# Kernel tuning notes

Measured on AMD Instinct MI355X. Metric: run time of the kernel, lower is better.

The kernel has to match this reference:

```python
import jax, jax.numpy as jnp
import numpy as np

TOKENS = 32768
DIM = 2048
N_EXPERTS = 64
TOP_K = 6
ROUTE_SCALE = 1.0


def setup_inputs() -> dict:
    key = jax.random.key(0)
    k1, k2, k3 = jax.random.split(key, 3)
    x = jax.random.normal(k1, (TOKENS, DIM), dtype=jnp.float32)
    weight = jax.random.normal(k2, (N_EXPERTS, DIM), dtype=jnp.float32) * (1.0 / np.sqrt(DIM))
    bias = jax.random.normal(k3, (N_EXPERTS,), dtype=jnp.float32) * 0.01
    return {"x": x, "weight": weight, "bias": bias}


def reference(x, weight, bias):
    # scores = F.linear(x, weight): [T, E]
    logits = jnp.einsum('td,ed->te', x, weight)
    # softmax in float32 (score_func == 'softmax')
    original_scores = jax.nn.softmax(logits.astype(jnp.float32), axis=-1)
    # bias only affects expert selection, not the returned weights
    biased = original_scores + bias
    _, indices = jax.lax.top_k(biased, TOP_K)  # [T, top_k]
    weights = jnp.take_along_axis(original_scores, indices, axis=-1)
    weights = weights * ROUTE_SCALE
    return weights.astype(x.dtype), indices
```

## Files before the change

kernel.cpp:

```cpp
#include <hip/hip_runtime.h>
#include <hip/hip_bf16.h>
#include <math.h>

#define TOKENS 32768
#define DIM    2048
#define NEXP   64
#define TOPK   6

#define BM   64
#define BK   64
#define NIT  (DIM / BK)
#define PL_SH   (NEXP * BK)
#define CH_SH   (3 * PL_SH)
#define CH_B    (CH_SH * 2)

typedef float f32x4 __attribute__((ext_vector_type(4)));
typedef short sh8  __attribute__((ext_vector_type(8)));

__device__ __forceinline__ ushort f2bf(float f) {
    union { __hip_bfloat16 b; ushort u; } c;
    c.b = __float2bfloat16(f);
    return c.u;
}
__device__ __forceinline__ float bf2f(ushort u) {
    union { ushort u; __hip_bfloat16 b; } c;
    c.u = u;
    return __bfloat162float(c.b);
}

#define GLDS(gp, lp) __builtin_amdgcn_global_load_lds( \
    (const __attribute__((address_space(1))) void*)(gp), \
    (__attribute__((address_space(3))) void*)(lp), 16, 0, 0)

__global__ void wsplit_kernel(const float* __restrict__ w, short* __restrict__ ws)
{
    const int idx = blockIdx.x * 256 + threadIdx.x;
    const int g  = idx & 7;
    const int e  = (idx >> 3) & 63;
    const int it = idx >> 9;
    const int c  = g ^ (e & 7);

    const float* src = w + (long)e * DIM + it * BK + c * 8;
    float4 f0 = *(const float4*)(src);
    float4 f1 = *(const float4*)(src + 4);

    sh8 h, m, l;
#pragma unroll
    for (int i = 0; i < 8; ++i) {
        float f = (i < 4) ? ((const float*)&f0)[i] : ((const float*)&f1)[i - 4];
        ushort hh = f2bf(f);  float r1 = f - bf2f(hh);
        ushort mm = f2bf(r1); float r2 = r1 - bf2f(mm);
        ushort ll = f2bf(r2);
        h[i] = (short)hh; m[i] = (short)mm; l[i] = (short)ll;
    }
    short* dst = ws + (long)it * CH_SH + e * BK + g * 8;
    *(sh8*)(dst)              = h;
    *(sh8*)(dst + PL_SH)      = m;
    *(sh8*)(dst + 2 * PL_SH)  = l;
}

__global__ __launch_bounds__(256, 2)
void gate_kernel(const float* __restrict__ x,
                 const short* __restrict__ ws,
                 const float* __restrict__ bias,
                 float* __restrict__ out)
{
    __shared__ __align__(16) short smem[2 * CH_SH];

    const int tid  = threadIdx.x;
    const int wave = tid >> 6;
    const int lane = tid & 63;
    const int quad = lane >> 4;
    const int l15  = lane & 15;
    const int tok0 = blockIdx.x * BM;

    const float* xg = x + (long)(tok0 + wave * 16 + l15) * DIM + quad * 8;

    const int h8  = l15 & 7;
    const int vb0 = l15 * 128 + (((0 * 4 + quad) ^ h8) << 4);
    const int vb1 = l15 * 128 + (((1 * 4 + quad) ^ h8) << 4);
    const char* sb = (const char*)smem;

    f32x4 acc[4];
#pragma unroll
    for (int nt = 0; nt < 4; ++nt) acc[nt] = (f32x4){0.f, 0.f, 0.f, 0.f};

    auto stage = [&](int it, int bp) {
        const short* s = ws + (long)it * CH_SH + tid * 8;
        short* d = smem + bp * CH_SH + tid * 8;
#pragma unroll
        for (int j = 0; j < 6; ++j) GLDS(s + j * 2048, d + j * 2048);
    };

    float4 fA[4], fB[4];
    auto loadA = [&](float4* f, int it) {
        const float* p = xg + it * BK;
        f[0] = *(const float4*)(p);
        f[1] = *(const float4*)(p + 4);
        f[2] = *(const float4*)(p + 32);
        f[3] = *(const float4*)(p + 36);
    };

    sh8 fr[2][3];
    auto convert = [&](const float4* f) {
#pragma unroll
        for (int ks = 0; ks < 2; ++ks) {
            sh8 h, m, l;
#pragma unroll
            for (int i = 0; i < 8; ++i) {
                float v = ((const float*)&f[ks * 2])[i];
                ushort hh = f2bf(v);  float r1 = v - bf2f(hh);
                ushort mm = f2bf(r1); float r2 = r1 - bf2f(mm);
                h[i] = (short)hh; m[i] = (short)mm; l[i] = (short)f2bf(r2);
            }
            fr[ks][0] = h; fr[ks][1] = m; fr[ks][2] = l;
        }
    };

    auto compute = [&](int bufbyte) {
#pragma unroll
        for (int ks = 0; ks < 2; ++ks) {
            const int va = (ks ? vb1 : vb0) + bufbyte;
#pragma unroll
            for (int nt = 0; nt < 4; ++nt) {
                const int ro = va + nt * 2048;
                sh8 bh = *(const sh8*)(sb + ro);
                sh8 bm = *(const sh8*)(sb + ro + 8192);
                sh8 bl = *(const sh8*)(sb + ro + 16384);
                acc[nt] = __builtin_amdgcn_mfma_f32_16x16x32_bf16(fr[ks][0], bh, acc[nt], 0, 0, 0);
                acc[nt] = __builtin_amdgcn_mfma_f32_16x16x32_bf16(fr[ks][1], bh, acc[nt], 0, 0, 0);
                acc[nt] = __builtin_amdgcn_mfma_f32_16x16x32_bf16(fr[ks][0], bm, acc[nt], 0, 0, 0);
                acc[nt] = __builtin_amdgcn_mfma_f32_16x16x32_bf16(fr[ks][2], bh, acc[nt], 0, 0, 0);
                acc[nt] = __builtin_amdgcn_mfma_f32_16x16x32_bf16(fr[ks][1], bm, acc[nt], 0, 0, 0);
                acc[nt] = __builtin_amdgcn_mfma_f32_16x16x32_bf16(fr[ks][0], bl, acc[nt], 0, 0, 0);
            }
        }
    };

    stage(0, 0);
    loadA(fA, 0);
    loadA(fB, 1);
    __syncthreads();

#pragma unroll 1
    for (int it = 0; it < NIT; it += 2) {
        stage(it + 1, 1);
        convert(fA);
        if (it + 2 < NIT) loadA(fA, it + 2);
        compute(0);
        __syncthreads();

        if (it + 2 < NIT) stage(it + 2, 0);
        convert(fB);
        if (it + 3 < NIT) loadA(fB, it + 3);
        compute(CH_B);
        __syncthreads();
    }

    float* red = (float*)smem;
#pragma unroll
    for (int nt = 0; nt < 4; ++nt)
#pragma unroll
        for (int j = 0; j < 4; ++j) {
            const int row = wave * 16 + quad * 4 + j;
            const int col = nt * 16 + l15;
            red[row * 69 + col] = acc[nt][j];
        }
    __syncthreads();

    {
        const int t = lane >> 2;
        const int s = lane & 3;
        const int row = wave * 16 + t;

        float lg[16];
#pragma unroll
        for (int i = 0; i < 16; ++i) lg[i] = red[row * 69 + s * 16 + i];

        float mx = lg[0];
#pragma unroll
        for (int i = 1; i < 16; ++i) mx = fmaxf(mx, lg[i]);
        mx = fmaxf(mx, __shfl_xor(mx, 1));
        mx = fmaxf(mx, __shfl_xor(mx, 2));

        float sum = 0.f;
#pragma unroll
        for (int i = 0; i < 16; ++i) { lg[i] = __expf(lg[i] - mx); sum += lg[i]; }
        sum += __shfl_xor(sum, 1);
        sum += __shfl_xor(sum, 2);
        const float inv = 1.0f / sum;

        float sc[16], bz[16];
#pragma unroll
        for (int i = 0; i < 16; ++i) {
            sc[i] = lg[i] * inv;
            bz[i] = sc[i] + bias[s * 16 + i];
        }

        const int tok = tok0 + wave * 16 + t;
        float* wout = out + (long)tok * TOPK;
        float* iout = out + (long)TOKENS * TOPK + (long)tok * TOPK;

        unsigned used = 0;
#pragma unroll
        for (int p = 0; p < TOPK; ++p) {
            float bv = -INFINITY; int bi = 1 << 20; float bw = 0.f;
#pragma unroll
            for (int i = 0; i < 16; ++i) {
                float v = ((used >> i) & 1u) ? -INFINITY : bz[i];
                if (v > bv) { bv = v; bi = s * 16 + i; bw = sc[i]; }
            }
#pragma unroll
            for (int d = 1; d < 4; d <<= 1) {
                float ov = __shfl_xor(bv, d);
                int   oi = __shfl_xor(bi, d);
                float ow = __shfl_xor(bw, d);
                if (ov > bv || (ov == bv && oi < bi)) { bv = ov; bi = oi; bw = ow; }
            }
            if ((bi >> 4) == s) used |= 1u << (bi & 15);
            if (s == 0) { wout[p] = bw; iout[p] = (float)bi; }
        }
    }
}

extern "C" void kernel_launch(void* const* d_in, const int* in_sizes, int n_in,
                              void* d_out, int out_size, void* d_ws, size_t ws_size,
                              hipStream_t stream) {
    const float* x = (const float*)d_in[0];
    const float* w = (const float*)d_in[1];
    const float* b = (const float*)d_in[2];
    float* out = (float*)d_out;
    short* ws = (short*)d_ws;

    wsplit_kernel<<<dim3(64), dim3(256), 0, stream>>>(w, ws);
    gate_kernel<<<dim3(TOKENS / BM), dim3(256), 0, stream>>>(x, ws, b, out);
}
```

Baseline: 382.5 us.

## Switch gate GEMM from 16x16x32 to 32x32x16 MFMA tiles

Each wave now computes a 32-token by 32-expert tile with the 32x32x16 bf16 MFMA instead of four 16x16 tiles along the expert dimension. The A-fragment loads, LDS B-fragment addressing and the accumulator scatter into the reduction buffer are remapped to the 32x32 layout. The aim is fewer MFMA issues and fewer LDS B-fragment reads per k-step, giving higher matrix-core efficiency. The cost is more A registers per thread (8 float4 per buffer) and possible LDS bank conflicts under the new swizzle.

```diff
diff --git a/kernel.cpp b/kernel.cpp
--- a/kernel.cpp
+++ b/kernel.cpp
@@ -14,7 +14,7 @@
 #define CH_SH   (3 * PL_SH)
 #define CH_B    (CH_SH * 2)
 
-typedef float f32x4 __attribute__((ext_vector_type(4)));
+typedef float f32x16 __attribute__((ext_vector_type(16)));
 typedef short sh8  __attribute__((ext_vector_type(8)));
 
 __device__ __forceinline__ ushort f2bf(float f) {
@@ -70,20 +70,27 @@
     const int tid  = threadIdx.x;
     const int wave = tid >> 6;
     const int lane = tid & 63;
-    const int quad = lane >> 4;
-    const int l15  = lane & 15;
     const int tok0 = blockIdx.x * BM;
 
-    const float* xg = x + (long)(tok0 + wave * 16 + l15) * DIM + quad * 8;
-
-    const int h8  = l15 & 7;
-    const int vb0 = l15 * 128 + (((0 * 4 + quad) ^ h8) << 4);
-    const int vb1 = l15 * 128 + (((1 * 4 + quad) ^ h8) << 4);
+    const int tt = wave >> 1;
+    const int et = wave & 1;
+    const int e5 = lane & 31;
+    const int hb = lane >> 5;
+    const int h3 = e5 & 7;
+
+    const float* xg = x + (long)(tok0 + tt * 32 + e5) * DIM + hb * 8;
+
+    const int ecol = et * 32 + e5;
+    const int eh3  = ecol & 7;
+    int vk[4];
+#pragma unroll
+    for (int ks = 0; ks < 4; ++ks)
+        vk[ks] = ecol * 128 + (((ks * 2 + hb) ^ eh3) << 4);
     const char* sb = (const char*)smem;
 
-    f32x4 acc[4];
-#pragma unroll
-    for (int nt = 0; nt < 4; ++nt) acc[nt] = (f32x4){0.f, 0.f, 0.f, 0.f};
+    f32x16 acc;
+#pragma unroll
+    for (int i = 0; i < 16; ++i) acc[i] = 0.f;
 
     auto stage = [&](int it, int bp) {
         const short* s = ws + (long)it * CH_SH + tid * 8;
@@ -92,19 +99,20 @@
         for (int j = 0; j < 6; ++j) GLDS(s + j * 2048, d + j * 2048);
     };
 
-    float4 fA[4], fB[4];
+    float4 fA[8], fB[8];
     auto loadA = [&](float4* f, int it) {
         const float* p = xg + it * BK;
-        f[0] = *(const float4*)(p);
-        f[1] = *(const float4*)(p + 4);
-        f[2] = *(const float4*)(p + 32);
-        f[3] = *(const float4*)(p + 36);
-    };
-
-    sh8 fr[2][3];
+#pragma unroll
+        for (int ks = 0; ks < 4; ++ks) {
+            f[2 * ks]     = *(const float4*)(p + ks * 16);
+            f[2 * ks + 1] = *(const float4*)(p + ks * 16 + 4);
+        }
+    };
+
+    sh8 fr[4][3];
     auto convert = [&](const float4* f) {
 #pragma unroll
-        for (int ks = 0; ks < 2; ++ks) {
+        for (int ks = 0; ks < 4; ++ks) {
             sh8 h, m, l;
 #pragma unroll
             for (int i = 0; i < 8; ++i) {
@@ -119,21 +127,17 @@
 
     auto compute = [&](int bufbyte) {
 #pragma unroll
-        for (int ks = 0; ks < 2; ++ks) {
-            const int va = (ks ? vb1 : vb0) + bufbyte;
-#pragma unroll
-            for (int nt = 0; nt < 4; ++nt) {
-                const int ro = va + nt * 2048;
-                sh8 bh = *(const sh8*)(sb + ro);
-                sh8 bm = *(const sh8*)(sb + ro + 8192);
-                sh8 bl = *(const sh8*)(sb + ro + 16384);
-                acc[nt] = __builtin_amdgcn_mfma_f32_16x16x32_bf16(fr[ks][0], bh, acc[nt], 0, 0, 0);
-                acc[nt] = __builtin_amdgcn_mfma_f32_16x16x32_bf16(fr[ks][1], bh, acc[nt], 0, 0, 0);
-                acc[nt] = __builtin_amdgcn_mfma_f32_16x16x32_bf16(fr[ks][0], bm, acc[nt], 0, 0, 0);
-                acc[nt] = __builtin_amdgcn_mfma_f32_16x16x32_bf16(fr[ks][2], bh, acc[nt], 0, 0, 0);
-                acc[nt] = __builtin_amdgcn_mfma_f32_16x16x32_bf16(fr[ks][1], bm, acc[nt], 0, 0, 0);
-                acc[nt] = __builtin_amdgcn_mfma_f32_16x16x32_bf16(fr[ks][0], bl, acc[nt], 0, 0, 0);
-            }
+        for (int ks = 0; ks < 4; ++ks) {
+            const int ro = vk[ks] + bufbyte;
+            sh8 bh = *(const sh8*)(sb + ro);
+            sh8 bm = *(const sh8*)(sb + ro + 8192);
+            sh8 bl = *(const sh8*)(sb + ro + 16384);
+            acc = __builtin_amdgcn_mfma_f32_32x32x16_bf16(fr[ks][0], bh, acc, 0, 0, 0);
+            acc = __builtin_amdgcn_mfma_f32_32x32x16_bf16(fr[ks][1], bh, acc, 0, 0, 0);
+            acc = __builtin_amdgcn_mfma_f32_32x32x16_bf16(fr[ks][0], bm, acc, 0, 0, 0);
+            acc = __builtin_amdgcn_mfma_f32_32x32x16_bf16(fr[ks][2], bh, acc, 0, 0, 0);
+            acc = __builtin_amdgcn_mfma_f32_32x32x16_bf16(fr[ks][1], bm, acc, 0, 0, 0);
+            acc = __builtin_amdgcn_mfma_f32_32x32x16_bf16(fr[ks][0], bl, acc, 0, 0, 0);
         }
     };
 
@@ -159,13 +163,12 @@
 
     float* red = (float*)smem;
 #pragma unroll
-    for (int nt = 0; nt < 4; ++nt)
-#pragma unroll
-        for (int j = 0; j < 4; ++j) {
-            const int row = wave * 16 + quad * 4 + j;
-            const int col = nt * 16 + l15;
-            red[row * 69 + col] = acc[nt][j];
-        }
+    for (int reg = 0; reg < 16; ++reg) {
+        const int r   = (reg & 3) + 8 * (reg >> 2) + 4 * hb;
+        const int row = tt * 32 + r;
+        const int col = et * 32 + e5;
+        red[row * 69 + col] = acc[reg];
+    }
     __syncthreads();
 
     {
```

New measurement: 387.9 us. About the same (+1.4%).
